# Performance work log

Hardware: AMD Instinct MI355X
Metric: run time of the kernel (lower is better)

The kernel has to match this reference:

```python
import jax, jax.numpy as jnp
import numpy as np

NS, BS, U, NR, NT, D = 256, 7, 8, 4, 8, 2
ITERS, HID = 3, 200
P, NOISE = 100.0, 1e-7
CIN = 2 * NT * D  # block input width: flattened Z1 and Z2


def setup_inputs() -> dict:
    key = jax.random.key(0)
    ks = jax.random.split(key, 21)
    rn = lambda k, s: jax.random.normal(k, s, dtype=jnp.float32)
    inp = {
        'H_re': rn(ks[0], (NS, BS, BS, U, NR, NT)),
        'H_im': rn(ks[1], (NS, BS, BS, U, NR, NT)),
        'V_re': rn(ks[2], (NS, BS, U, NT, D)),
        'V_im': rn(ks[3], (NS, BS, U, NT, D)),
        'w': jnp.ones((U,), jnp.float32),
        'W1_re': rn(ks[4], (ITERS, HID, CIN)) * 0.05,
        'W1_im': rn(ks[5], (ITERS, HID, CIN)) * 0.05,
        'b1_re': rn(ks[6], (ITERS, HID)) * 0.05,
        'b1_im': rn(ks[7], (ITERS, HID)) * 0.05,
        'W2_re': rn(ks[8], (ITERS, HID, HID)) * 0.05,
        'W2_im': rn(ks[9], (ITERS, HID, HID)) * 0.05,
        'b2_re': rn(ks[10], (ITERS, HID)) * 0.05,
        'b2_im': rn(ks[11], (ITERS, HID)) * 0.05,
        'W3_re': rn(ks[12], (ITERS, HID, HID)) * 0.05,
        'W3_im': rn(ks[13], (ITERS, HID, HID)) * 0.05,
        'b3_re': rn(ks[14], (ITERS, HID)) * 0.05,
        'b3_im': rn(ks[15], (ITERS, HID)) * 0.05,
        'W4_re': rn(ks[16], (ITERS, 1, HID)) * 0.05,
        'W4_im': rn(ks[17], (ITERS, 1, HID)) * 0.05,
        'b4_re': rn(ks[18], (ITERS, 1)) * 0.05,
        'b4_im': rn(ks[19], (ITERS, 1)) * 0.05,
    }
    return inp


def _crelu(x):
    # ComplexReLU: relu on real part, imaginary part passes through
    return jax.nn.relu(x.real) + 1j * x.imag


def _clin(x, W, b):
    # torch Linear with complex weights: x @ W.T + b
    return jnp.einsum('...i,oi->...o', x, W) + b


def _iteration(H, V, w, p):
    n = H.shape[0]
    Z = V
    # HV[n,k,l,i,j] = H[n,k,l,i] @ V[n,k,j]  -> [n,BS,BS,U,U,NR,D]
    HV = jnp.einsum('nklirt,nkjtd->nklijrd', H, V)
    ab = jnp.arange(BS)
    au = jnp.arange(U)
    HV2 = HV[:, ab, ab][:, :, au, au]  # HV[:,k,k,i,i] -> [n,BS,U,NR,D]
    # T[n,k,l,i,j] = HV @ HV^H -> [n,BS,BS,U,U,NR,NR]
    T = jnp.einsum('nklijrd,nklijsd->nklijrs', HV, HV.conj())
    I_r = jnp.eye(NR, dtype=HV.dtype)
    # U[n,l,u] = noise*I + sum_{k,j} T[n,k,l,u,j]
    Usum = NOISE * I_r + T.sum(axis=(1, 4))  # [n,BS,U,NR,NR]
    Y = jnp.linalg.solve(Usum, HV2)
    Td = T[:, ab, ab][:, :, au, au]  # T[:,l,l,u,u]
    F = Usum - Td
    Gamma = jnp.einsum('nlurd,nlure->nlude', HV2.conj(), jnp.linalg.solve(F, HV2))
    IG = jnp.eye(D, dtype=HV.dtype) + Gamma  # [n,BS,U,D,D]
    # A[n,l,m,u] = H[n,l,m,u].mH @ Y[n,m,u] -> [n,BS,BS,U,NT,D]
    A = jnp.einsum('nlmurt,nmurd->nlmutd', H.conj(), Y)
    # L[n,l,u] = sum_m A @ IG[m,u] @ A^H -> [n,BS,U,NT,NT]
    L = jnp.einsum('nlmutd,nmude,nlmuse->nluts', A, IG, A.conj())
    All = A[:, ab, ab]  # A[:,l,l] -> [n,BS,U,NT,D]
    Lam = jnp.einsum('nlutd,nlude->nlute', All, IG)
    wv = w.astype(HV.dtype)[None, None, :, None, None]
    Lam = Lam * wv
    L = L * wv
    Z2 = Lam - jnp.einsum('nluts,nlusd->nlutd', L, Z)
    inp = jnp.concatenate([Z.reshape(n, BS, U, NT * D), Z2.reshape(n, BS, U, NT * D)], -1)
    W1, b1, W2, b2, W3, b3, W4, b4 = p
    h = _crelu(_clin(inp, W1, b1))
    h = _crelu(_clin(h, W2, b2))
    h = _crelu(_clin(h, W3, b3))
    step = _clin(h, W4, b4).real  # [n,BS,U,1]
    Vn = Z + step[..., None] * Z2
    fro = (jnp.abs(Vn) ** 2).sum((-2, -1)).sum(2)  # [n,BS]
    scale = jnp.where(fro > P, jnp.sqrt(P / fro), 1.0)
    return Vn * scale[:, :, None, None, None].astype(Vn.dtype)


def reference(H_re, H_im, V_re, V_im, w, W1_re, W1_im, b1_re, b1_im, W2_re, W2_im, b2_re, b2_im, W3_re, W3_im, b3_re, b3_im, W4_re, W4_im, b4_re, b4_im):
    H = (H_re + 1j * H_im).astype(jnp.complex64)
    V = (V_re + 1j * V_im).astype(jnp.complex64)
    # init_input power normalization per (sample, BS)
    fro0 = (jnp.abs(V) ** 2).sum((-2, -1)).sum(2)
    V = V * jnp.sqrt(P / fro0)[:, :, None, None, None].astype(V.dtype)
    c64 = jnp.complex64
    Ws = [(W1_re + 1j * W1_im).astype(c64), (b1_re + 1j * b1_im).astype(c64),
          (W2_re + 1j * W2_im).astype(c64), (b2_re + 1j * b2_im).astype(c64),
          (W3_re + 1j * W3_im).astype(c64), (b3_re + 1j * b3_im).astype(c64),
          (W4_re + 1j * W4_im).astype(c64), (b4_re + 1j * b4_im).astype(c64)]
    for it in range(ITERS):
        p = tuple(a[it] for a in Ws)
        V = _iteration(H, V, w, p)
    return jnp.stack([V.real, V.imag], axis=-1)
```

## Files before the change

### kernel.cpp

```cpp
#include <hip/hip_runtime.h>
#include <math.h>

#define NS 256
#define BS 7
#define UU 8
#define NR 4
#define NT 8
#define DD 2
#define HID 200
#define CIN 32
#define PP 100.0f
#define NOISEF 1e-7f

typedef _Float16 f16x8 __attribute__((ext_vector_type(8)));
typedef float f32x4 __attribute__((ext_vector_type(4)));

#define AST 424
#define AST0 104
#define NTILES 28
#define B1_KC 3
#define B23_KC 13
#define B1_HALVES (B1_KC*NTILES*64*8)
#define B23_HALVES (B23_KC*NTILES*64*8)
#define BITER_HALVES (B1_HALVES + 2*B23_HALVES)

__device__ void chol_solve(const float2 (*A)[NR], const float2 (*B)[DD], float2 (*X)[DD]) {
  float2 L[NR][NR];
  for (int j = 0; j < NR; ++j) {
    float d = A[j][j].x;
    for (int k = 0; k < j; ++k) d -= L[j][k].x * L[j][k].x + L[j][k].y * L[j][k].y;
    float ld = sqrtf(fmaxf(d, 1e-30f));
    L[j][j] = make_float2(ld, 0.f);
    float inv = 1.f / ld;
    for (int i = j + 1; i < NR; ++i) {
      float sr = A[i][j].x, si = A[i][j].y;
      for (int k = 0; k < j; ++k) {
        float2 a = L[i][k], b = L[j][k];
        sr -= a.x * b.x + a.y * b.y;
        si -= a.y * b.x - a.x * b.y;
      }
      L[i][j] = make_float2(sr * inv, si * inv);
    }
  }
  for (int c = 0; c < DD; ++c) {
    float2 z[NR];
    for (int i = 0; i < NR; ++i) {
      float sr = B[i][c].x, si = B[i][c].y;
      for (int k = 0; k < i; ++k) {
        float2 a = L[i][k], zz = z[k];
        sr -= a.x * zz.x - a.y * zz.y;
        si -= a.x * zz.y + a.y * zz.x;
      }
      float inv = 1.f / L[i][i].x;
      z[i] = make_float2(sr * inv, si * inv);
    }
    for (int i = NR - 1; i >= 0; --i) {
      float sr = z[i].x, si = z[i].y;
      for (int k = i + 1; k < NR; ++k) {
        float2 a = L[k][i], xx = X[k][c];
        sr -= a.x * xx.x + a.y * xx.y;
        si -= a.x * xx.y - a.y * xx.x;
      }
      float inv = 1.f / L[i][i].x;
      X[i][c] = make_float2(sr * inv, si * inv);
    }
  }
}

__global__ void k_norm0(const float* __restrict__ Vre, const float* __restrict__ Vim,
                        float2* __restrict__ Vcur) {
  int nl = blockIdx.x;
  int tid = threadIdx.x;
  size_t base = (size_t)nl * 128;
  float re = Vre[base + tid], im = Vim[base + tid];
  float p = re * re + im * im;
  p += __shfl_down(p, 32); p += __shfl_down(p, 16); p += __shfl_down(p, 8);
  p += __shfl_down(p, 4);  p += __shfl_down(p, 2);  p += __shfl_down(p, 1);
  __shared__ float sred[2];
  if ((tid & 63) == 0) sred[tid >> 6] = p;
  __syncthreads();
  float fro = sred[0] + sred[1];
  float sc = sqrtf(PP / fro);
  Vcur[base + tid] = make_float2(re * sc, im * sc);
}

__global__ __launch_bounds__(448) void k_C(const float2* __restrict__ Vcur,
    float2* __restrict__ Cb) {
  int n = blockIdx.x;
  int tid = threadIdx.x;
  __shared__ float2 Vs[952];
  const float2* Vn = Vcur + (size_t)n * 896;
  for (int idx = tid; idx < 896; idx += 448)
    Vs[(idx >> 4) * 17 + (idx & 15)] = Vn[idx];
  __syncthreads();
  int k = tid >> 6, e = tid & 63, c = e >> 3, t = e & 7;
  float sr = 0.f, si = 0.f;
  #pragma unroll
  for (int j = 0; j < 8; ++j) {
    const float2* vr = &Vs[(k * 8 + j) * 17];
    #pragma unroll
    for (int d = 0; d < 2; ++d) {
      float2 a = vr[t * 2 + d], b = vr[c * 2 + d];
      sr += a.x * b.x + a.y * b.y;
      si += a.y * b.x - a.x * b.y;
    }
  }
  Cb[((size_t)(n * 7 + k) * 8 + c) * 8 + t] = make_float2(sr, si);
}

__global__ __launch_bounds__(64) void k_gpart(const float* __restrict__ Hre,
    const float* __restrict__ Him, const float2* __restrict__ Vcur,
    const float2* __restrict__ Cb, float2* __restrict__ Gpart,
    float2* __restrict__ Tdb, float2* __restrict__ HV2b) {
  int blk = blockIdx.x;
  int k = blk % 7; int l = (blk / 7) % 7; int n = blk / 49;
  int lane = threadIdx.x;
  int i = lane >> 3, c = lane & 7;
  size_t b_nli = (size_t)n * 56 + l * 8 + i;

  size_t hoff = (((size_t)(n * 7 + k) * 7 + l) * 8 + i) * 32;
  float hx[4][8], hy[4][8];
  #pragma unroll
  for (int r = 0; r < 4; ++r) {
    float4 a0 = *(const float4*)(Hre + hoff + r * 8);
    float4 a1 = *(const float4*)(Hre + hoff + r * 8 + 4);
    float4 b0 = *(const float4*)(Him + hoff + r * 8);
    float4 b1 = *(const float4*)(Him + hoff + r * 8 + 4);
    hx[r][0] = a0.x; hx[r][1] = a0.y; hx[r][2] = a0.z; hx[r][3] = a0.w;
    hx[r][4] = a1.x; hx[r][5] = a1.y; hx[r][6] = a1.z; hx[r][7] = a1.w;
    hy[r][0] = b0.x; hy[r][1] = b0.y; hy[r][2] = b0.z; hy[r][3] = b0.w;
    hy[r][4] = b1.x; hy[r][5] = b1.y; hy[r][6] = b1.z; hy[r][7] = b1.w;
  }
  float2 Hc[4];
  #pragma unroll
  for (int s = 0; s < 4; ++s)
    Hc[s] = make_float2(Hre[hoff + s * 8 + c], Him[hoff + s * 8 + c]);

  const float2* ct = Cb + ((size_t)(n * 7 + k) * 8 + c) * 8;
  float2 cc[8];
  #pragma unroll
  for (int t2 = 0; t2 < 4; ++t2) {
    float4 vv = *(const float4*)(ct + t2 * 2);
    cc[t2 * 2]     = make_float2(vv.x, vv.y);
    cc[t2 * 2 + 1] = make_float2(vv.z, vv.w);
  }

  float2 T[4];
  #pragma unroll
  for (int r = 0; r < 4; ++r) {
    float tr = 0.f, ti = 0.f;
    #pragma unroll
    for (int t = 0; t < 8; ++t) {
      tr += hx[r][t] * cc[t].x - hy[r][t] * cc[t].y;
      ti += hx[r][t] * cc[t].y + hy[r][t] * cc[t].x;
    }
    T[r] = make_float2(tr, ti);
  }
  float2 G[10];
  {
    int ui = 0;
    #pragma unroll
    for (int r = 0; r < 4; ++r)
      #pragma unroll
      for (int s = r; s < 4; ++s) {
        float2 a = T[r], hb = Hc[s];
        G[ui].x = a.x * hb.x + a.y * hb.y;
        G[ui].y = a.y * hb.x - a.x * hb.y;
        ++ui;
      }
  }
  #pragma unroll
  for (int m = 1; m < 8; m <<= 1) {
    #pragma unroll
    for (int q = 0; q < 10; ++q) {
      G[q].x += __shfl_xor(G[q].x, m);
      G[q].y += __shfl_xor(G[q].y, m);
    }
  }
  if (c == 0) {
    float2* gp = Gpart + (b_nli * 7 + k) * 10;
    #pragma unroll
    for (int q = 0; q < 10; ++q) gp[q] = G[q];
  }

  if (k == l) {
    const float2* vp = Vcur + b_nli * 16;
    float2 v[8][2];
    #pragma unroll
    for (int q = 0; q < 8; ++q) {
      float4 vv = *(const float4*)(vp + 2 * q);
      v[q][0] = make_float2(vv.x, vv.y);
      v[q][1] = make_float2(vv.z, vv.w);
    }
    float2 hv[4][2];
    #pragma unroll
    for (int r = 0; r < 4; ++r)
      #pragma unroll
      for (int d = 0; d < 2; ++d) {
        float ar = 0.f, ai = 0.f;
        #pragma unroll
        for (int t = 0; t < 8; ++t) {
          ar += hx[r][t] * v[t][d].x - hy[r][t] * v[t][d].y;
          ai += hx[r][t] * v[t][d].y + hy[r][t] * v[t][d].x;
        }
        hv[r][d] = make_float2(ar, ai);
      }
    if (c == 0) {
      float2* tdp = Tdb + b_nli * 10;
      int ui = 0;
      #pragma unroll
      for (int r = 0; r < 4; ++r)
        #pragma unroll
        for (int s = r; s < 4; ++s) {
          float tr = 0.f, ti = 0.f;
          #pragma unroll
          for (int d = 0; d < 2; ++d) {
            float2 a = hv[r][d], cx = hv[s][d];
            tr += a.x * cx.x + a.y * cx.y;
            ti += a.y * cx.x - a.x * cx.y;
          }
          tdp[ui] = make_float2(tr, ti);
          ++ui;
        }
      float2* h2p = HV2b + b_nli * 8;
      #pragma unroll
      for (int x = 0; x < 8; ++x) h2p[x] = hv[x >> 1][x & 1];
    }
  }
}

__global__ __launch_bounds__(256) void k_solveR(const float2* __restrict__ Gpart,
    const float2* __restrict__ Tdb, const float2* __restrict__ HV2b,
    float2* __restrict__ Yb, float2* __restrict__ IGb) {
  int gid = blockIdx.x * 256 + threadIdx.x;
  int which = (gid >= 14336) ? 1 : 0;
  int b = gid - which * 14336;

  float2 G[10];
  #pragma unroll
  for (int q = 0; q < 10; ++q) G[q] = make_float2(0.f, 0.f);
  const float2* gp = Gpart + (size_t)b * 70;
  #pragma unroll
  for (int k = 0; k < 7; ++k)
    #pragma unroll
    for (int q = 0; q < 10; ++q) {
      float2 g = gp[k * 10 + q];
      G[q].x += g.x; G[q].y += g.y;
    }
  if (which) {
    const float2* tp = Tdb + (size_t)b * 10;
    #pragma unroll
    for (int q = 0; q < 10; ++q) { float2 t = tp[q]; G[q].x -= t.x; G[q].y -= t.y; }
  }
  float2 M[NR][NR];
  {
    int ui = 0;
    #pragma unroll
    for (int r = 0; r < 4; ++r)
      #pragma unroll
      for (int s = r; s < 4; ++s) {
        M[r][s] = G[ui];
        M[s][r] = make_float2(G[ui].x, -G[ui].y);
        ++ui;
      }
    #pragma unroll
    for (int r = 0; r < 4; ++r) { M[r][r].x += NOISEF; M[r][r].y = 0.f; }
  }
  float2 Bv[NR][DD], X[NR][DD];
  const float2* hp = HV2b + (size_t)b * 8;
  #pragma unroll
  for (int x = 0; x < 8; ++x) Bv[x >> 1][x & 1] = hp[x];
  chol_solve(M, Bv, X);
  if (!which) {
    #pragma unroll
    for (int x = 0; x < 8; ++x) Yb[(size_t)b * 8 + x] = X[x >> 1][x & 1];
  } else {
    #pragma unroll
    for (int d = 0; d < DD; ++d)
      #pragma unroll
      for (int e = 0; e < DD; ++e) {
        float gr = (d == e) ? 1.f : 0.f, gi = 0.f;
        #pragma unroll
        for (int r = 0; r < NR; ++r) {
          float2 a = Bv[r][d], x = X[r][e];
          gr += a.x * x.x + a.y * x.y;
          gi += a.x * x.y - a.y * x.x;
        }
        IGb[(size_t)b * 4 + d * 2 + e] = make_float2(gr, gi);
      }
  }
}

__global__ __launch_bounds__(256) void k_stage2(const float* __restrict__ Hre,
    const float* __restrict__ Him, const float2* __restrict__ Vcur,
    const float2* __restrict__ Yb, const float2* __restrict__ IGb,
    const float* __restrict__ w, float2* __restrict__ Z2out) {
  int nl = blockIdx.x; int l = nl % BS; int n = nl / BS;
  int tid = threadIdx.x;
  __shared__ float2 SM[3686];
  float2* Hsm  = SM;
  float2* Bsm  = SM;
  float2* Lsm  = SM + 952;
  float2* Ysm  = SM + 1792;
  float2* IGsm = SM + 2247;
  float2* Asm  = SM + 2478;
  float2* Lamm = SM + 3430;
  float2* Zlm  = SM + 3558;

  size_t hbase = ((size_t)n * BS + l) * 1792;
  for (int idx = tid; idx < 1792; idx += 256) {
    int t = idx & 7, r = (idx >> 3) & 3, u = (idx >> 5) & 7, m = idx >> 8;
    Hsm[((u * 4 + r) * 7 + m) * 8 + t] = make_float2(Hre[hbase + idx], Him[hbase + idx]);
  }
  const float2* yp = Yb + (size_t)n * 448;
  for (int idx = tid; idx < 448; idx += 256)
    Ysm[(idx >> 6) * 65 + (idx & 63)] = yp[idx];
  const float2* igp = IGb + (size_t)n * 224;
  if (tid < 224) IGsm[(tid >> 5) * 33 + (tid & 31)] = igp[tid];
  const float2* zp = Vcur + (size_t)nl * 128;
  if (tid < 128) Zlm[tid] = zp[tid];
  __syncthreads();

  for (int idx = tid; idx < 896; idx += 256) {
    int u = idx / 112, rem = idx % 112, m = rem >> 4, t = (rem >> 1) & 7, d = rem & 1;
    float ar = 0.f, ai = 0.f;
    #pragma unroll
    for (int r = 0; r < NR; ++r) {
      float2 h = Hsm[((u * 4 + r) * 7 + m) * 8 + t];
      float2 y = Ysm[m * 65 + u * 8 + r * 2 + d];
      ar += h.x * y.x + h.y * y.y;
      ai += h.x * y.y - h.y * y.x;
    }
    Asm[u * 119 + m * 17 + t * 2 + d] = make_float2(ar, ai);
  }
  __syncthreads();

  for (int idx = tid; idx < 896; idx += 256) {
    int u = idx / 112, rem = idx % 112, m = rem >> 4, t = (rem >> 1) & 7, e = rem & 1;
    float br = 0.f, bi = 0.f;
    #pragma unroll
    for (int d = 0; d < DD; ++d) {
      float2 a = Asm[u * 119 + m * 17 + t * 2 + d];
      float2 g = IGsm[m * 33 + u * 4 + d * 2 + e];
      br += a.x * g.x - a.y * g.y;
      bi += a.x * g.y + a.y * g.x;
    }
    Bsm[u * 119 + m * 17 + t * 2 + e] = make_float2(br, bi);
  }
  __syncthreads();

  for (int idx = tid; idx < 512; idx += 256) {
    int u = idx >> 6, t = (idx >> 3) & 7, s = idx & 7;
    float lr = 0.f, li = 0.f;
    #pragma unroll
    for (int m = 0; m < BS; ++m)
      #pragma unroll
      for (int e = 0; e < DD; ++e) {
        float2 bb = Bsm[u * 119 + m * 17 + t * 2 + e];
        float2 ac = Asm[u * 119 + m * 17 + s * 2 + e];
        lr += bb.x * ac.x + bb.y * ac.y;
        li += bb.y * ac.x - bb.x * ac.y;
      }
    float wu = w[u];
    Lsm[(u * 8 + t) * 8 + s] = make_float2(lr * wu, li * wu);
  }
  if (tid < 128) {
    int u = tid >> 4, t = (tid >> 1) & 7, e = tid & 1;
    float ar = 0.f, ai = 0.f;
    #pragma unroll
    for (int d = 0; d < DD; ++d) {
      float2 a = Asm[u * 119 + l * 17 + t * 2 + d];
      float2 g = IGsm[l * 33 + u * 4 + d * 2 + e];
      ar += a.x * g.x - a.y * g.y;
      ai += a.x * g.y + a.y * g.x;
    }
    float wu = w[u];
    Lamm[u * 16 + t * 2 + e] = make_float2(ar * wu, ai * wu);
  }
  __syncthreads();

  if (tid < 128) {
    int u = tid >> 4, t = (tid >> 1) & 7, d = tid & 1;
    float2 lam = Lamm[u * 16 + t * 2 + d];
    float zr = lam.x, zi = lam.y;
    #pragma unroll
    for (int s = 0; s < NT; ++s) {
      float2 Lts = Lsm[(u * 8 + t) * 8 + s];
      float2 z = Zlm[u * 16 + s * 2 + d];
      zr -= Lts.x * z.x - Lts.y * z.y;
      zi -= Lts.x * z.y + Lts.y * z.x;
    }
    Z2out[(size_t)nl * 128 + u * 16 + t * 2 + d] = make_float2(zr, zi);
  }
}

__global__ __launch_bounds__(256) void k_pack(
    const float* __restrict__ W1re, const float* __restrict__ W1im,
    const float* __restrict__ b1re, const float* __restrict__ b1im,
    const float* __restrict__ W2re, const float* __restrict__ W2im,
    const float* __restrict__ b2re, const float* __restrict__ b2im,
    const float* __restrict__ W3re, const float* __restrict__ W3im,
    const float* __restrict__ b3re, const float* __restrict__ b3im,
    _Float16* __restrict__ Bout) {
  int gid = blockIdx.x * 256 + threadIdx.x;
  int lane = gid & 63;
  int rest = gid >> 6;
  int nt = rest % NTILES;
  int id2 = rest / NTILES;
  if (id2 >= 87) return;
  int iter = id2 / 29, kk = id2 % 29;
  int layer, kc;
  if (kk < 3)       { layer = 0; kc = kk; }
  else if (kk < 16) { layer = 1; kc = kk - 3; }
  else              { layer = 2; kc = kk - 16; }
  const float *Wr, *Wi, *br, *bi;
  if (layer == 0) { Wr = W1re + iter*HID*CIN; Wi = W1im + iter*HID*CIN; br = b1re + iter*HID; bi = b1im + iter*HID; }
  else if (layer == 1) { Wr = W2re + iter*HID*HID; Wi = W2im + iter*HID*HID; br = b2re + iter*HID; bi = b2im + iter*HID; }
  else { Wr = W3re + iter*HID*HID; Wi = W3im + iter*HID*HID; br = b3re + iter*HID; bi = b3im + iter*HID; }
  int c = nt * 16 + (lane & 15);
  int o = c >> 1; int odd = c & 1;
  f16x8 frag;
  #pragma unroll
  for (int j = 0; j < 8; ++j) {
    int k = kc * 32 + (lane >> 4) * 8 + j;
    float v = 0.f;
    if (o < HID) {
      if (layer == 0) {
        if (k < 32)       v = odd ? Wi[o*32 + k] : Wr[o*32 + k];
        else if (k < 64)  { int i = k - 32; v = odd ? Wr[o*32 + i] : -Wi[o*32 + i]; }
        else if (k == 64) v = odd ? bi[o] : br[o];
      } else {
        if (k < 200)       v = odd ? Wi[o*200 + k] : Wr[o*200 + k];
        else if (k == 207) v = odd ? bi[o] : br[o];
        else if (k >= 208 && k < 408) { int i = k - 208; v = odd ? Wr[o*200 + i] : -Wi[o*200 + i]; }
      }
    }
    frag[j] = (_Float16)v;
  }
  size_t off = (size_t)iter * BITER_HALVES
             + (layer == 0 ? 0 : (layer == 1 ? B1_HALVES : (B1_HALVES + B23_HALVES)))
             + ((size_t)(kc * NTILES + nt) * 64 + lane) * 8;
  *(f16x8*)(Bout + off) = frag;
}

template<int ASTRIDE, int KC>
__device__ inline void do_gemm(const _Float16* Ain,
                               const _Float16* __restrict__ Bg,
                               _Float16* Aout, int wr, int wc, int lane) {
  f32x4 acc[2][7];
  #pragma unroll
  for (int rt = 0; rt < 2; ++rt)
    #pragma unroll
    for (int nt = 0; nt < 7; ++nt)
      acc[rt][nt] = (f32x4){0.f, 0.f, 0.f, 0.f};
  const int r0 = (lane & 15) + wr * 32, g = lane >> 4;
  const _Float16* bp0 = Bg + ((size_t)(wc * 7) * 64 + lane) * 8;
  f16x8 b[7];
  #pragma unroll
  for (int nt = 0; nt < 7; ++nt) b[nt] = *(const f16x8*)(bp0 + nt * 512);
  f16x8 a0 = *(const f16x8*)(Ain + r0 * ASTRIDE + 8 * g);
  f16x8 a1 = *(const f16x8*)(Ain + (r0 + 16) * ASTRIDE + 8 * g);
  #pragma unroll
  for (int kc = 0; kc < KC; ++kc) {
    f16x8 a0n, a1n, bn[7];
    if (kc + 1 < KC) {
      const _Float16* bpn = bp0 + (size_t)(kc + 1) * (NTILES * 512);
      #pragma unroll
      for (int nt = 0; nt < 7; ++nt) bn[nt] = *(const f16x8*)(bpn + nt * 512);
      a0n = *(const f16x8*)(Ain + r0 * ASTRIDE + (kc + 1) * 32 + 8 * g);
      a1n = *(const f16x8*)(Ain + (r0 + 16) * ASTRIDE + (kc + 1) * 32 + 8 * g);
    }
    #pragma unroll
    for (int nt = 0; nt < 7; ++nt) {
      acc[0][nt] = __builtin_amdgcn_mfma_f32_16x16x32_f16(a0, b[nt], acc[0][nt], 0, 0, 0);
      acc[1][nt] = __builtin_amdgcn_mfma_f32_16x16x32_f16(a1, b[nt], acc[1][nt], 0, 0, 0);
    }
    if (kc + 1 < KC) {
      a0 = a0n; a1 = a1n;
      #pragma unroll
      for (int nt = 0; nt < 7; ++nt) b[nt] = bn[nt];
    }
  }
  int cbase = wc * 7 * 16 + (lane & 15);
  #pragma unroll
  for (int nt = 0; nt < 7; ++nt) {
    int c = cbase + nt * 16;
    int o = c >> 1;
    bool isre = !(c & 1);
    if (o < HID) {
      _Float16* outp = Aout + (isre ? o : 208 + o);
      #pragma unroll
      for (int rt = 0; rt < 2; ++rt)
        #pragma unroll
        for (int q = 0; q < 4; ++q) {
          float v = acc[rt][nt][q];
          if (isre) v = fmaxf(v, 0.f);
          outp[(size_t)(wr * 32 + rt * 16 + g * 4 + q) * AST] = (_Float16)v;
        }
    }
  }
}

__global__ __launch_bounds__(512, 2) void k_mlp_mfma(
    const float2* __restrict__ Vcur, const float2* __restrict__ Z2,
    const _Float16* __restrict__ Bp,
    const float* __restrict__ W4re, const float* __restrict__ W4im,
    const float* __restrict__ b4re,
    float2* __restrict__ Vout) {
  int b = blockIdx.x;
  int tid = threadIdx.x;
  int wave = tid >> 6, lane = tid & 63;
  int wr = wave >> 2, wc = wave & 3;

  __shared__ _Float16 A0[64 * AST0];
  __shared__ _Float16 Abuf[2][64 * AST];
  __shared__ float2 Zs[64][16];
  __shared__ float2 Z2s[64][16];
  __shared__ float w4s[2][HID];
  __shared__ float stepv[64];
  __shared__ float scs[8];

  for (int idx = tid; idx < 1024; idx += 512) {
    ((float2*)Zs)[idx]  = Vcur[(size_t)b * 1024 + idx];
    ((float2*)Z2s)[idx] = Z2[(size_t)b * 1024 + idx];
  }
  for (int idx = tid; idx < HID; idx += 512) {
    w4s[0][idx] = W4re[idx];
    w4s[1][idx] = W4im[idx];
  }
  __syncthreads();

  for (int idx = tid; idx < 64 * AST0; idx += 512) {
    int m = idx / AST0, c = idx % AST0;
    float v;
    if (c < 64) {
      int f = c & 31;
      float2 z = (f < 16) ? Zs[m][f] : Z2s[m][f - 16];
      v = (c >= 32) ? z.y : z.x;
    } else v = (c == 64) ? 1.f : 0.f;
    A0[m * AST0 + c] = (_Float16)v;
  }
  for (int idx = tid; idx < 2 * 64 * 16; idx += 512) {
    int buf = idx >> 10, rem = idx & 1023, m = rem >> 4, p = rem & 15;
    int c = (p < 8) ? (200 + p) : (400 + p);
    Abuf[buf][m * AST + c] = (p == 7) ? (_Float16)1.f : (_Float16)0.f;
  }
  __syncthreads();

  do_gemm<AST0, B1_KC>(A0, Bp, &Abuf[0][0], wr, wc, lane);
  __syncthreads();
  do_gemm<AST, B23_KC>(&Abuf[0][0], Bp + B1_HALVES, &Abuf[1][0], wr, wc, lane);
  __syncthreads();
  do_gemm<AST, B23_KC>(&Abuf[1][0], Bp + B1_HALVES + B23_HALVES, &Abuf[0][0], wr, wc, lane);
  __syncthreads();

  {
    int m = tid >> 3, q = tid & 7;
    float acc = 0.f;
    for (int o = q; o < HID; o += 8) {
      float hr = (float)Abuf[0][m * AST + o];
      float hi = (float)Abuf[0][m * AST + 208 + o];
      acc += hr * w4s[0][o] - hi * w4s[1][o];
    }
    acc += __shfl_down(acc, 4, 8);
    acc += __shfl_down(acc, 2, 8);
    acc += __shfl_down(acc, 1, 8);
    if (q == 0) stepv[m] = acc + b4re[0];
  }
  __syncthreads();

  for (int idx = tid; idx < 1024; idx += 512) {
    int m = idx >> 4, f = idx & 15;
    float st = stepv[m];
    float2 z = Zs[m][f], z2 = Z2s[m][f];
    Zs[m][f] = make_float2(fmaf(st, z2.x, z.x), fmaf(st, z2.y, z.y));
  }
  __syncthreads();

  {
    const float2* vp = &Zs[wave * 8][0];
    float2 v0 = vp[lane * 2], v1 = vp[lane * 2 + 1];
    float p = v0.x * v0.x + v0.y * v0.y + v1.x * v1.x + v1.y * v1.y;
    p += __shfl_down(p, 32); p += __shfl_down(p, 16); p += __shfl_down(p, 8);
    p += __shfl_down(p, 4);  p += __shfl_down(p, 2);  p += __shfl_down(p, 1);
    if (lane == 0) scs[wave] = (p > PP) ? sqrtf(PP / p) : 1.f;
  }
  __syncthreads();
  for (int idx = tid; idx < 1024; idx += 512) {
    float sc = scs[idx >> 7];
    float2 v = ((float2*)Zs)[idx];
    Vout[(size_t)b * 1024 + idx] = make_float2(v.x * sc, v.y * sc);
  }
}

extern "C" void kernel_launch(void* const* d_in, const int* in_sizes, int n_in,
                              void* d_out, int out_size, void* d_ws, size_t ws_size,
                              hipStream_t stream) {
  const float* Hre  = (const float*)d_in[0];
  const float* Him  = (const float*)d_in[1];
  const float* Vre  = (const float*)d_in[2];
  const float* Vim  = (const float*)d_in[3];
  const float* w    = (const float*)d_in[4];
  const float* W1re = (const float*)d_in[5];
  const float* W1im = (const float*)d_in[6];
  const float* b1re = (const float*)d_in[7];
  const float* b1im = (const float*)d_in[8];
  const float* W2re = (const float*)d_in[9];
  const float* W2im = (const float*)d_in[10];
  const float* b2re = (const float*)d_in[11];
  const float* b2im = (const float*)d_in[12];
  const float* W3re = (const float*)d_in[13];
  const float* W3im = (const float*)d_in[14];
  const float* b3re = (const float*)d_in[15];
  const float* b3im = (const float*)d_in[16];
  const float* W4re = (const float*)d_in[17];
  const float* W4im = (const float*)d_in[18];
  const float* b4re = (const float*)d_in[19];

  const size_t NV = (size_t)NS * BS * UU * NT * DD;
  const size_t NB = (size_t)NS * BS * UU;
  float2* Vcur = (float2*)d_ws;
  float2* Z2b  = Vcur + NV;
  float2* Yb   = Z2b + NV;
  float2* IGb  = Yb + NB * 8;
  float2* Cb   = IGb + NB * 4;
  float2* Gpart= Cb + (size_t)NS * 7 * 64;
  float2* Tdb  = Gpart + NB * 70;
  float2* HV2b = Tdb + NB * 10;
  _Float16* Bpack = (_Float16*)(HV2b + NB * 8);

  k_pack<<<609, 256, 0, stream>>>(W1re, W1im, b1re, b1im, W2re, W2im, b2re, b2im,
                                  W3re, W3im, b3re, b3im, Bpack);
  k_norm0<<<NS * BS, 128, 0, stream>>>(Vre, Vim, Vcur);
  for (int it = 0; it < 3; ++it) {
    k_C<<<NS, 448, 0, stream>>>(Vcur, Cb);
    k_gpart<<<NS * BS * BS, 64, 0, stream>>>(Hre, Him, Vcur, Cb, Gpart, Tdb, HV2b);
    k_solveR<<<112, 256, 0, stream>>>(Gpart, Tdb, HV2b, Yb, IGb);
    k_stage2<<<NS * BS, 256, 0, stream>>>(Hre, Him, Vcur, Yb, IGb, w, Z2b);
    float2* vout = (it == 2) ? (float2*)d_out : Vcur;
    k_mlp_mfma<<<NS * BS / 8, 512, 0, stream>>>(Vcur, Z2b,
        Bpack + (size_t)it * BITER_HALVES,
        W4re + it * HID, W4im + it * HID, b4re + it, vout);
  }
}
```

Measured before the change: 246.4 us.

## Partition MLP GEMM by column tiles so each wave covers all rows

Each of the 8 waves now computes every 64 rows for its own 4 or 3 column tiles, instead of a 2x4 grid where each wave covered 32 rows by 7 tiles. Each wave now loads only its own B weight fragments from global memory, cutting redundant weight traffic, while A reads from shared memory go up to 4 row tiles per wave. The explicit register double-buffered prefetch of A and B is removed and scheduling is left to the compiler, which may expose load latency. The uneven 4/3 tile split leaves some waves with less work.

```diff
diff --git a/kernel.cpp b/kernel.cpp
--- a/kernel.cpp
+++ b/kernel.cpp
@@ -443,59 +443,48 @@
   *(f16x8*)(Bout + off) = frag;
 }
 
-template<int ASTRIDE, int KC>
+template<int ASTRIDE, int KC, int NTL>
 __device__ inline void do_gemm(const _Float16* Ain,
                                const _Float16* __restrict__ Bg,
-                               _Float16* Aout, int wr, int wc, int lane) {
-  f32x4 acc[2][7];
-  #pragma unroll
-  for (int rt = 0; rt < 2; ++rt)
-    #pragma unroll
-    for (int nt = 0; nt < 7; ++nt)
+                               _Float16* Aout, int tbase, int lane) {
+  f32x4 acc[4][NTL];
+  #pragma unroll
+  for (int rt = 0; rt < 4; ++rt)
+    #pragma unroll
+    for (int nt = 0; nt < NTL; ++nt)
       acc[rt][nt] = (f32x4){0.f, 0.f, 0.f, 0.f};
-  const int r0 = (lane & 15) + wr * 32, g = lane >> 4;
-  const _Float16* bp0 = Bg + ((size_t)(wc * 7) * 64 + lane) * 8;
-  f16x8 b[7];
-  #pragma unroll
-  for (int nt = 0; nt < 7; ++nt) b[nt] = *(const f16x8*)(bp0 + nt * 512);
-  f16x8 a0 = *(const f16x8*)(Ain + r0 * ASTRIDE + 8 * g);
-  f16x8 a1 = *(const f16x8*)(Ain + (r0 + 16) * ASTRIDE + 8 * g);
+  const int r0 = lane & 15, g = lane >> 4;
+  const _Float16* bp0 = Bg + ((size_t)tbase * 64 + lane) * 8;
+  const size_t KSTEP = (size_t)NTILES * 512;
   #pragma unroll
   for (int kc = 0; kc < KC; ++kc) {
-    f16x8 a0n, a1n, bn[7];
-    if (kc + 1 < KC) {
-      const _Float16* bpn = bp0 + (size_t)(kc + 1) * (NTILES * 512);
-      #pragma unroll
-      for (int nt = 0; nt < 7; ++nt) bn[nt] = *(const f16x8*)(bpn + nt * 512);
-      a0n = *(const f16x8*)(Ain + r0 * ASTRIDE + (kc + 1) * 32 + 8 * g);
-      a1n = *(const f16x8*)(Ain + (r0 + 16) * ASTRIDE + (kc + 1) * 32 + 8 * g);
-    }
-    #pragma unroll
-    for (int nt = 0; nt < 7; ++nt) {
-      acc[0][nt] = __builtin_amdgcn_mfma_f32_16x16x32_f16(a0, b[nt], acc[0][nt], 0, 0, 0);
-      acc[1][nt] = __builtin_amdgcn_mfma_f32_16x16x32_f16(a1, b[nt], acc[1][nt], 0, 0, 0);
-    }
-    if (kc + 1 < KC) {
-      a0 = a0n; a1 = a1n;
-      #pragma unroll
-      for (int nt = 0; nt < 7; ++nt) b[nt] = bn[nt];
-    }
-  }
-  int cbase = wc * 7 * 16 + (lane & 15);
-  #pragma unroll
-  for (int nt = 0; nt < 7; ++nt) {
-    int c = cbase + nt * 16;
+    f16x8 b[NTL], a[4];
+    #pragma unroll
+    for (int nt = 0; nt < NTL; ++nt)
+      b[nt] = *(const f16x8*)(bp0 + (size_t)kc * KSTEP + nt * 512);
+    #pragma unroll
+    for (int rt = 0; rt < 4; ++rt)
+      a[rt] = *(const f16x8*)(Ain + (r0 + rt * 16) * ASTRIDE + kc * 32 + 8 * g);
+    #pragma unroll
+    for (int nt = 0; nt < NTL; ++nt)
+      #pragma unroll
+      for (int rt = 0; rt < 4; ++rt)
+        acc[rt][nt] = __builtin_amdgcn_mfma_f32_16x16x32_f16(a[rt], b[nt], acc[rt][nt], 0, 0, 0);
+  }
+  #pragma unroll
+  for (int nt = 0; nt < NTL; ++nt) {
+    int c = (tbase + nt) * 16 + r0;
     int o = c >> 1;
     bool isre = !(c & 1);
     if (o < HID) {
       _Float16* outp = Aout + (isre ? o : 208 + o);
       #pragma unroll
-      for (int rt = 0; rt < 2; ++rt)
+      for (int rt = 0; rt < 4; ++rt)
         #pragma unroll
         for (int q = 0; q < 4; ++q) {
           float v = acc[rt][nt][q];
           if (isre) v = fmaxf(v, 0.f);
-          outp[(size_t)(wr * 32 + rt * 16 + g * 4 + q) * AST] = (_Float16)v;
+          outp[(size_t)(rt * 16 + g * 4 + q) * AST] = (_Float16)v;
         }
     }
   }
@@ -510,7 +499,7 @@
   int b = blockIdx.x;
   int tid = threadIdx.x;
   int wave = tid >> 6, lane = tid & 63;
-  int wr = wave >> 2, wc = wave & 3;
+  int tb = (wave < 4) ? wave * 4 : 16 + (wave - 4) * 3;
 
   __shared__ _Float16 A0[64 * AST0];
   __shared__ _Float16 Abuf[2][64 * AST];
@@ -547,11 +536,14 @@
   }
   __syncthreads();
 
-  do_gemm<AST0, B1_KC>(A0, Bp, &Abuf[0][0], wr, wc, lane);
-  __syncthreads();
-  do_gemm<AST, B23_KC>(&Abuf[0][0], Bp + B1_HALVES, &Abuf[1][0], wr, wc, lane);
-  __syncthreads();
-  do_gemm<AST, B23_KC>(&Abuf[1][0], Bp + B1_HALVES + B23_HALVES, &Abuf[0][0], wr, wc, lane);
+  if (wave < 4) do_gemm<AST0, B1_KC, 4>(A0, Bp, &Abuf[0][0], tb, lane);
+  else          do_gemm<AST0, B1_KC, 3>(A0, Bp, &Abuf[0][0], tb, lane);
+  __syncthreads();
+  if (wave < 4) do_gemm<AST, B23_KC, 4>(&Abuf[0][0], Bp + B1_HALVES, &Abuf[1][0], tb, lane);
+  else          do_gemm<AST, B23_KC, 3>(&Abuf[0][0], Bp + B1_HALVES, &Abuf[1][0], tb, lane);
+  __syncthreads();
+  if (wave < 4) do_gemm<AST, B23_KC, 4>(&Abuf[1][0], Bp + B1_HALVES + B23_HALVES, &Abuf[0][0], tb, lane);
+  else          do_gemm<AST, B23_KC, 3>(&Abuf[1][0], Bp + B1_HALVES + B23_HALVES, &Abuf[0][0], tb, lane);
   __syncthreads();
 
   {
```

New measurement: 245.0 us. No clear change (-0.6%).
